# Kernel tuning notes

Measured on AMD Instinct MI355X. Metric: run time of the kernel, lower is better.

Reference implementation:

```python
import jax, jax.numpy as jnp
import numpy as np

N, DEG, IN_DIM, OUT_DIM = 50000, 32, 128, 64
NEG_SLOPE = 0.01  # F.leaky_relu default


def setup_inputs() -> dict:
    key = jax.random.key(0)
    k1, k2, k3, k4 = jax.random.split(key, 4)
    feature = jax.random.normal(k1, (N, IN_DIM), dtype=jnp.float32)
    src_idx = jax.random.randint(k2, (N, DEG), 0, N)
    fc_weight = jax.random.uniform(k3, (IN_DIM, OUT_DIM), dtype=jnp.float32)
    attn_weight = jax.random.uniform(k4, (2 * OUT_DIM, 1), dtype=jnp.float32)
    return {"feature": feature, "src_idx": src_idx,
            "fc_weight": fc_weight, "attn_weight": attn_weight}


def reference(feature, src_idx, fc_weight, attn_weight):
    out_dim = fc_weight.shape[1]
    # message: z = h_src @ W  (compute per-node once, then gather per edge)
    z = feature @ fc_weight                       # [N, D]
    z_src = z[src_idx]                            # [N, deg, D] mailbox 'z'
    # a = concat(z_src, z_dst) @ attn  ==  z_src @ a[:D] + z_dst @ a[D:]
    a_src = (z_src @ attn_weight[:out_dim])[..., 0]   # [N, deg]
    a_dst = z @ attn_weight[out_dim:]                 # [N, 1]
    e = jax.nn.leaky_relu(a_src + a_dst, NEG_SLOPE)   # [N, deg] mailbox 'e'
    # reduce: alpha[n, j] = sum_k relu(e[n, j] - e[n, k])
    alpha = jnp.sum(jnp.maximum(e[:, :, None] - e[:, None, :], 0.0), axis=2)  # [N, deg]
    # h[n] = sum_j alpha[n, j] * z_src[n, j]
    h = jnp.einsum('nd,ndo->no', alpha, z_src)    # [N, D]
    return h
```

## Files before the change

### kernel.cpp

```cpp
#include <hip/hip_runtime.h>

#define IN_DIM  128
#define OUT_DIM 64
#define DEG     32
#define NEG_SLOPE 0.01f

typedef __attribute__((ext_vector_type(8))) short  short8;
typedef __attribute__((ext_vector_type(4))) float  f32x4;

__device__ __forceinline__ unsigned short f2bf(float x) {
    unsigned u = __float_as_uint(x);
    unsigned r = u + 0x7FFFu + ((u >> 16) & 1u);
    return (unsigned short)(r >> 16);
}
__device__ __forceinline__ float bf2f(unsigned short b) {
    return __uint_as_float(((unsigned)b) << 16);
}

__global__ __launch_bounds__(256) void cgat_fc(
    const float* __restrict__ feat,
    const float* __restrict__ W,
    const float* __restrict__ aw,
    unsigned short* __restrict__ zb,
    float* __restrict__ s,
    float* __restrict__ t,
    int n)
{
    const int lane = threadIdx.x & 63;
    const int hi   = lane >> 4;
    const int lo   = lane & 15;

    short8 Bh[4][4], Bl[4][4];
    #pragma unroll
    for (int kt = 0; kt < 4; ++kt) {
        #pragma unroll
        for (int nt = 0; nt < 4; ++nt) {
            #pragma unroll
            for (int j = 0; j < 8; ++j) {
                const float w = W[(kt * 32 + hi * 8 + j) * OUT_DIM + nt * 16 + lo];
                const unsigned short h = f2bf(w);
                Bh[kt][nt][j] = (short)h;
                Bl[kt][nt][j] = (short)f2bf(w - bf2f(h));
            }
        }
    }

    float aw_s[4], aw_t[4];
    #pragma unroll
    for (int nt = 0; nt < 4; ++nt) {
        aw_s[nt] = aw[nt * 16 + lo];
        aw_t[nt] = aw[OUT_DIM + nt * 16 + lo];
    }

    const int wave   = blockIdx.x * 4 + (threadIdx.x >> 6);
    const int nwaves = gridDim.x * 4;
    const int njobs  = (n + 15) >> 4;

    for (int job = wave; job < njobs; job += nwaves) {
        int r0 = job << 4;
        if (r0 + 16 > n) r0 = (n >= 16) ? (n - 16) : 0;
        const float* frow = feat + (size_t)(r0 + lo) * IN_DIM + hi * 8;

        f32x4 acc[4] = {{0,0,0,0},{0,0,0,0},{0,0,0,0},{0,0,0,0}};

        #pragma unroll
        for (int kt = 0; kt < 4; ++kt) {
            const float4 a0 = *(const float4*)(frow + kt * 32);
            const float4 a1 = *(const float4*)(frow + kt * 32 + 4);
            const float av[8] = {a0.x, a0.y, a0.z, a0.w, a1.x, a1.y, a1.z, a1.w};
            short8 Ah, Al;
            #pragma unroll
            for (int j = 0; j < 8; ++j) {
                const unsigned short h = f2bf(av[j]);
                Ah[j] = (short)h;
                Al[j] = (short)f2bf(av[j] - bf2f(h));
            }
            #pragma unroll
            for (int nt = 0; nt < 4; ++nt) {
                acc[nt] = __builtin_amdgcn_mfma_f32_16x16x32_bf16(Ah, Bh[kt][nt], acc[nt], 0, 0, 0);
                acc[nt] = __builtin_amdgcn_mfma_f32_16x16x32_bf16(Ah, Bl[kt][nt], acc[nt], 0, 0, 0);
                acc[nt] = __builtin_amdgcn_mfma_f32_16x16x32_bf16(Al, Bh[kt][nt], acc[nt], 0, 0, 0);
            }
        }

        #pragma unroll
        for (int reg = 0; reg < 4; ++reg) {
            const int row = r0 + 4 * hi + reg;
            float sv = 0.f, tv = 0.f;
            #pragma unroll
            for (int nt = 0; nt < 4; ++nt) {
                const float v = acc[nt][reg];
                zb[(size_t)row * OUT_DIM + nt * 16 + lo] = f2bf(v);
                sv = fmaf(v, aw_s[nt], sv);
                tv = fmaf(v, aw_t[nt], tv);
            }
            #pragma unroll
            for (int off = 8; off > 0; off >>= 1) {
                sv += __shfl_xor(sv, off, 64);
                tv += __shfl_xor(tv, off, 64);
            }
            if (lo == 0) { s[row] = sv; t[row] = tv; }
        }
    }
}

__global__ __launch_bounds__(256) void cgat_gather(
    const int*   __restrict__ idx,
    const unsigned short* __restrict__ zb,
    const float* __restrict__ s,
    const float* __restrict__ t,
    float* __restrict__ h,
    int n)
{
    const int lane = threadIdx.x & 63;
    int node = blockIdx.x * 4 + (threadIdx.x >> 6);
    if (node >= n) return;
    node = __builtin_amdgcn_readfirstlane(node);

    const float tn = t[node];

    int   ij = 0;
    float e  = 0.f;
    if (lane < DEG) {
        ij = idx[(size_t)node * DEG + lane];
        e  = s[ij] + tn;
        e  = (e >= 0.f) ? e : NEG_SLOPE * e;
    }

    float al0 = 0.f, al1 = 0.f, al2 = 0.f, al3 = 0.f;
    #pragma unroll
    for (int k = 0; k < DEG; k += 4) {
        const float e0 = __int_as_float(__builtin_amdgcn_readlane(__float_as_int(e), k + 0));
        const float e1 = __int_as_float(__builtin_amdgcn_readlane(__float_as_int(e), k + 1));
        const float e2 = __int_as_float(__builtin_amdgcn_readlane(__float_as_int(e), k + 2));
        const float e3 = __int_as_float(__builtin_amdgcn_readlane(__float_as_int(e), k + 3));
        al0 += fmaxf(e - e0, 0.f);
        al1 += fmaxf(e - e1, 0.f);
        al2 += fmaxf(e - e2, 0.f);
        al3 += fmaxf(e - e3, 0.f);
    }
    const float alpha = (al0 + al1) + (al2 + al3);

    float h0 = 0.f, h1 = 0.f, h2 = 0.f, h3 = 0.f;
    #pragma unroll
    for (int k = 0; k < DEG; k += 4) {
        const float a0 = __int_as_float(__builtin_amdgcn_readlane(__float_as_int(alpha), k + 0));
        const float a1 = __int_as_float(__builtin_amdgcn_readlane(__float_as_int(alpha), k + 1));
        const float a2 = __int_as_float(__builtin_amdgcn_readlane(__float_as_int(alpha), k + 2));
        const float a3 = __int_as_float(__builtin_amdgcn_readlane(__float_as_int(alpha), k + 3));
        const int   i0 = __builtin_amdgcn_readlane(ij, k + 0);
        const int   i1 = __builtin_amdgcn_readlane(ij, k + 1);
        const int   i2 = __builtin_amdgcn_readlane(ij, k + 2);
        const int   i3 = __builtin_amdgcn_readlane(ij, k + 3);
        h0 = fmaf(a0, bf2f(zb[(size_t)i0 * OUT_DIM + lane]), h0);
        h1 = fmaf(a1, bf2f(zb[(size_t)i1 * OUT_DIM + lane]), h1);
        h2 = fmaf(a2, bf2f(zb[(size_t)i2 * OUT_DIM + lane]), h2);
        h3 = fmaf(a3, bf2f(zb[(size_t)i3 * OUT_DIM + lane]), h3);
    }
    h[(size_t)node * OUT_DIM + lane] = (h0 + h1) + (h2 + h3);
}

extern "C" void kernel_launch(void* const* d_in, const int* in_sizes, int n_in,
                              void* d_out, int out_size, void* d_ws, size_t ws_size,
                              hipStream_t stream)
{
    const float* feat = (const float*)d_in[0];
    const int*   idx  = (const int*)  d_in[1];
    const float* W    = (const float*)d_in[2];
    const float* aw   = (const float*)d_in[3];
    float*       h    = (float*)d_out;

    const int n = in_sizes[0] / IN_DIM;

    float* s = (float*)d_ws;
    float* t = s + n;
    unsigned short* zb = (unsigned short*)(t + n);

    cgat_fc<<<512, 256, 0, stream>>>(feat, W, aw, zb, s, t, n);

    const int ga_blocks = (n + 3) / 4;
    cgat_gather<<<ga_blocks, 256, 0, stream>>>(idx, zb, s, t, h, n);
}
```

Baseline: 120.1 us.

## Process two nodes per wavefront in gather kernel with packed bf16 loads

Result: no change. 118.6 us (-1.2%).

```diff
diff --git a/kernel.cpp b/kernel.cpp
--- a/kernel.cpp
+++ b/kernel.cpp
@@ -113,27 +113,25 @@
     int n)
 {
     const int lane = threadIdx.x & 63;
-    int node = blockIdx.x * 4 + (threadIdx.x >> 6);
-    if (node >= n) return;
-    node = __builtin_amdgcn_readfirstlane(node);
+    const int l    = lane & 31;
+    const int hb   = lane & 32;
 
+    int node = (blockIdx.x * 4 + (threadIdx.x >> 6)) * 2 + (lane >> 5);
+    if (node >= n) node = n - 1;
+
+    const int   ij = idx[(size_t)node * DEG + l];
     const float tn = t[node];
 
-    int   ij = 0;
-    float e  = 0.f;
-    if (lane < DEG) {
-        ij = idx[(size_t)node * DEG + lane];
-        e  = s[ij] + tn;
-        e  = (e >= 0.f) ? e : NEG_SLOPE * e;
-    }
+    float e = s[ij] + tn;
+    e = (e >= 0.f) ? e : NEG_SLOPE * e;
 
     float al0 = 0.f, al1 = 0.f, al2 = 0.f, al3 = 0.f;
     #pragma unroll
     for (int k = 0; k < DEG; k += 4) {
-        const float e0 = __int_as_float(__builtin_amdgcn_readlane(__float_as_int(e), k + 0));
-        const float e1 = __int_as_float(__builtin_amdgcn_readlane(__float_as_int(e), k + 1));
-        const float e2 = __int_as_float(__builtin_amdgcn_readlane(__float_as_int(e), k + 2));
-        const float e3 = __int_as_float(__builtin_amdgcn_readlane(__float_as_int(e), k + 3));
+        const float e0 = __shfl(e, hb | (k + 0), 64);
+        const float e1 = __shfl(e, hb | (k + 1), 64);
+        const float e2 = __shfl(e, hb | (k + 2), 64);
+        const float e3 = __shfl(e, hb | (k + 3), 64);
         al0 += fmaxf(e - e0, 0.f);
         al1 += fmaxf(e - e1, 0.f);
         al2 += fmaxf(e - e2, 0.f);
@@ -141,23 +139,26 @@
     }
     const float alpha = (al0 + al1) + (al2 + al3);
 
-    float h0 = 0.f, h1 = 0.f, h2 = 0.f, h3 = 0.f;
+    const unsigned* __restrict__ zw = (const unsigned*)zb;
+    float h0a = 0.f, h0b = 0.f, h1a = 0.f, h1b = 0.f;
     #pragma unroll
-    for (int k = 0; k < DEG; k += 4) {
-        const float a0 = __int_as_float(__builtin_amdgcn_readlane(__float_as_int(alpha), k + 0));
-        const float a1 = __int_as_float(__builtin_amdgcn_readlane(__float_as_int(alpha), k + 1));
-        const float a2 = __int_as_float(__builtin_amdgcn_readlane(__float_as_int(alpha), k + 2));
-        const float a3 = __int_as_float(__builtin_amdgcn_readlane(__float_as_int(alpha), k + 3));
-        const int   i0 = __builtin_amdgcn_readlane(ij, k + 0);
-        const int   i1 = __builtin_amdgcn_readlane(ij, k + 1);
-        const int   i2 = __builtin_amdgcn_readlane(ij, k + 2);
-        const int   i3 = __builtin_amdgcn_readlane(ij, k + 3);
-        h0 = fmaf(a0, bf2f(zb[(size_t)i0 * OUT_DIM + lane]), h0);
-        h1 = fmaf(a1, bf2f(zb[(size_t)i1 * OUT_DIM + lane]), h1);
-        h2 = fmaf(a2, bf2f(zb[(size_t)i2 * OUT_DIM + lane]), h2);
-        h3 = fmaf(a3, bf2f(zb[(size_t)i3 * OUT_DIM + lane]), h3);
+    for (int k = 0; k < DEG; k += 2) {
+        const float a0 = __shfl(alpha, hb | (k + 0), 64);
+        const int   i0 = __shfl(ij,    hb | (k + 0), 64);
+        const float a1 = __shfl(alpha, hb | (k + 1), 64);
+        const int   i1 = __shfl(ij,    hb | (k + 1), 64);
+        const unsigned w0 = zw[(size_t)i0 * (OUT_DIM / 2) + l];
+        const unsigned w1 = zw[(size_t)i1 * (OUT_DIM / 2) + l];
+        h0a = fmaf(a0, __uint_as_float(w0 << 16), h0a);
+        h0b = fmaf(a0, __uint_as_float(w0 & 0xFFFF0000u), h0b);
+        h1a = fmaf(a1, __uint_as_float(w1 << 16), h1a);
+        h1b = fmaf(a1, __uint_as_float(w1 & 0xFFFF0000u), h1b);
     }
-    h[(size_t)node * OUT_DIM + lane] = (h0 + h1) + (h2 + h3);
+
+    float2 out;
+    out.x = h0a + h1a;
+    out.y = h0b + h1b;
+    *(float2*)(h + (size_t)node * OUT_DIM + 2 * l) = out;
 }
 
 extern "C" void kernel_launch(void* const* d_in, const int* in_sizes, int n_in,
@@ -178,6 +179,6 @@
 
     cgat_fc<<<512, 256, 0, stream>>>(feat, W, aw, zb, s, t, n);
 
-    const int ga_blocks = (n + 3) / 4;
+    const int ga_blocks = (n + 7) / 8;
     cgat_gather<<<ga_blocks, 256, 0, stream>>>(idx, zb, s, t, h, n);
 }
```
